# Performance work log

Measured on AMD Instinct MI355X. Metric: run time of the kernel, lower is better.

The kernel has to match this reference:

```python
import jax, jax.numpy as jnp
import numpy as np

WINDOW = 128
LOOK_BACKWARD = 1
LOOK_FORWARD = 0
PAD_VALUE = -1


def look_around(x, backward=LOOK_BACKWARD, forward=LOOK_FORWARD, pad_value=PAD_VALUE):
    # x: [b, windows, window_size, ...]; pad along windows axis, concat along window_size axis
    pad_width = [(0, 0)] * x.ndim
    pad_width[1] = (backward, forward)
    px = jnp.pad(x, pad_width, constant_values=pad_value)
    w = x.shape[1]
    return jnp.concatenate([px[:, i:i + w] for i in range(forward + backward + 1)], axis=2)


def rotate_half(x):
    x1, x2 = jnp.split(x, 2, axis=-1)
    return jnp.concatenate([-x2, x1], axis=-1)


def setup_inputs() -> dict:
    key = jax.random.key(0)
    k1, k2, k3 = jax.random.split(key, 3)
    B, H, N, D = 4, 16, 4096, 64
    return {
        "q": jax.random.normal(k1, (B, H, N, D), dtype=jnp.float32),
        "k": jax.random.normal(k2, (B, H, N, D), dtype=jnp.float32),
        "v": jax.random.normal(k3, (B, H, N, D), dtype=jnp.float32),
    }


def reference(q, k, v):
    B, H, N, D = q.shape
    qf = q.reshape(B * H, N, D)
    kf = k.reshape(B * H, N, D)
    vf = v.reshape(B * H, N, D)

    # --- inline rotary (SinusoidalEmbeddings + apply_rotary_pos_emb) ---
    inv_freq = 1.0 / (10000.0 ** (jnp.arange(0, D, 2, dtype=jnp.float32) / D))  # [D/2]
    t = jnp.arange(N, dtype=jnp.float32)
    half = t[:, None] * inv_freq[None, :]                      # [N, D/2]
    freqs = jnp.concatenate([half, half], axis=-1)             # [N, D]
    cos, sin = jnp.cos(freqs), jnp.sin(freqs)
    qf = qf * cos + rotate_half(qf) * sin
    kf = kf * cos + rotate_half(kf) * sin

    # --- blocked local attention ---
    w = WINDOW
    windows = N // w
    scale = D ** -0.5
    bq = qf.reshape(B * H, windows, w, D)
    bk = look_around(kf.reshape(B * H, windows, w, D))         # [bh, windows, j, D]
    bv = look_around(vf.reshape(B * H, windows, w, D))

    seq = jnp.arange(N).reshape(1, windows, w)
    bq_t = seq[..., :, None]                                   # [1, windows, w, 1]
    bq_k = look_around(seq)[..., None, :]                      # [1, windows, 1, j]

    sim = jnp.einsum('bwie,bwje->bwij', bq, bk) * scale        # [bh, windows, w, j]
    mask_value = -jnp.finfo(sim.dtype).max
    sim = jnp.where(bq_t < bq_k, mask_value, sim)              # causal mask

    attn = jax.nn.softmax(sim, axis=-1)
    out = jnp.einsum('bwij,bwje->bwie', attn, bv)              # [bh, windows, w, D]
    return out.reshape(B, H, N, D)
```

## Files before the change

### kernel.cpp

```cpp
#include <hip/hip_runtime.h>

typedef __attribute__((ext_vector_type(8))) short  short8;
typedef __attribute__((ext_vector_type(4))) short  short4v;
typedef __attribute__((ext_vector_type(4))) float  float4v;

#define MFMA_QK(A,B,C) __builtin_amdgcn_mfma_f32_16x16x32_bf16(A,B,C,0,0,0)
#define MFMA_PV(A,B,C) __builtin_amdgcn_mfma_f32_16x16x16bf16_1k(A,B,C,0,0,0)

static __device__ __forceinline__ short f2bf(float x) {
  unsigned u = __float_as_uint(x);
  u += 0x7fffu + ((u >> 16) & 1u);
  return (short)(u >> 16);
}

static __device__ __forceinline__ void rope_sc(float rev, float& sn, float& cs) {
  float fr = rev - floorf(rev);
  sn = __builtin_amdgcn_sinf(fr);
  cs = __builtin_amdgcn_cosf(fr);
}

static __device__ __forceinline__ float invfreq_rev(int idx) {
  return exp2f(-0.41524101186092034f * (float)idx) * 0.15915494309189535f;
}

#define N_ 4096
#define D_ 64
#define W_ 128

__global__ __launch_bounds__(512, 4)
void la_fused(const float* __restrict__ qg, const float* __restrict__ kg,
              const float* __restrict__ vg, float* __restrict__ outg)
{
  __shared__ __attribute__((aligned(16))) short Kl[256][72];
  __shared__ __attribute__((aligned(16))) short Vl[64][260];

  const int blk  = blockIdx.x;
  const int w    = blk & 31;
  const int bh   = blk >> 5;
  const int base = bh * (N_ * D_);
  const int tid  = threadIdx.x;

  {
    const float* kb = kg + base;
    const float* vb = vg + base;
#pragma unroll
    for (int it = 0; it < 4; ++it) {
      const int tau = it * 512 + tid;
      const int j   = tau >> 3;
      const int d0  = (tau & 7) << 2;
      const int g   = w * W_ - W_ + j;
      float klo[4], khi[4], vlo[4], vhi[4];
      if (g < 0) {
#pragma unroll
        for (int dd = 0; dd < 4; ++dd) { klo[dd]=khi[dd]=vlo[dd]=vhi[dd] = -1.0f; }
      } else {
        float4v a   = *(const float4v*)(kb + g * D_ + d0);
        float4v b   = *(const float4v*)(kb + g * D_ + d0 + 32);
        float4v va  = *(const float4v*)(vb + g * D_ + d0);
        float4v vb2 = *(const float4v*)(vb + g * D_ + d0 + 32);
        const float t = (float)g;
#pragma unroll
        for (int dd = 0; dd < 4; ++dd) {
          float sn, cs; rope_sc(t * invfreq_rev(d0 + dd), sn, cs);
          klo[dd] = a[dd] * cs - b[dd] * sn;
          khi[dd] = b[dd] * cs + a[dd] * sn;
          vlo[dd] = va[dd]; vhi[dd] = vb2[dd];
        }
      }
      short4v k0 = { f2bf(klo[0]), f2bf(klo[1]), f2bf(klo[2]), f2bf(klo[3]) };
      short4v k1 = { f2bf(khi[0]), f2bf(khi[1]), f2bf(khi[2]), f2bf(khi[3]) };
      *(short4v*)&Kl[j][d0]      = k0;
      *(short4v*)&Kl[j][d0 + 32] = k1;
      const int j4  = j >> 2;
      const int jlo = j & 3;
#pragma unroll
      for (int dd = 0; dd < 4; ++dd) {
        const int r0 = d0 + dd, r1 = r0 + 32;
        Vl[r0][((j4 ^ (r0 >> 4)) << 2) | jlo] = f2bf(vlo[dd]);
        Vl[r1][((j4 ^ (r1 >> 4)) << 2) | jlo] = f2bf(vhi[dd]);
      }
    }
  }
  __syncthreads();

  const int lane = tid & 63;
  const int wv   = tid >> 6;
  const int il   = lane & 15;
  const int qd   = lane >> 4;
  const int rw   = wv * 16 + il;

  short8 qf0, qf1;
  {
    const int n = w * W_ + rw;
    const float* qr = qg + base + n * D_ + qd * 8;
    float4v x0 = *(const float4v*)(qr);
    float4v x1 = *(const float4v*)(qr + 4);
    float4v y0 = *(const float4v*)(qr + 32);
    float4v y1 = *(const float4v*)(qr + 36);
    float lo[8], hi[8];
    const float t = (float)n;
#pragma unroll
    for (int jj = 0; jj < 8; ++jj) {
      const int d = qd * 8 + jj;
      float xx = (jj < 4) ? x0[jj & 3] : x1[jj & 3];
      float yy = (jj < 4) ? y0[jj & 3] : y1[jj & 3];
      float sn, cs; rope_sc(t * invfreq_rev(d), sn, cs);
      lo[jj] = xx * cs - yy * sn;
      hi[jj] = yy * cs + xx * sn;
    }
    qf0 = short8{ f2bf(lo[0]),f2bf(lo[1]),f2bf(lo[2]),f2bf(lo[3]),
                  f2bf(lo[4]),f2bf(lo[5]),f2bf(lo[6]),f2bf(lo[7]) };
    qf1 = short8{ f2bf(hi[0]),f2bf(hi[1]),f2bf(hi[2]),f2bf(hi[3]),
                  f2bf(hi[4]),f2bf(hi[5]),f2bf(hi[6]),f2bf(hi[7]) };
  }

  float4v O[4];
#pragma unroll
  for (int dt = 0; dt < 4; ++dt) { float4v z = {0.f,0.f,0.f,0.f}; O[dt] = z; }
  float sum = 0.f;
  const int tq = wv + 9;

#pragma unroll
  for (int t = 0; t < 16; ++t) if (t < tq) {
    const short8 a0 = *(const short8*)&Kl[t * 16 + il][qd * 8];
    const short8 a1 = *(const short8*)&Kl[t * 16 + il][32 + qd * 8];
    float4v S = {0.f, 0.f, 0.f, 0.f};
    S = MFMA_QK(a0, qf0, S);
    S = MFMA_QK(a1, qf1, S);
    float p[4];
#pragma unroll
    for (int r = 0; r < 4; ++r) {
      const int j = t * 16 + qd * 4 + r;
      float e = __expf(S[r] * 0.125f);
      p[r] = (j > rw + 128) ? 0.f : e;
      sum += p[r];
    }
    const short4v Pt = short4v{ f2bf(p[0]), f2bf(p[1]), f2bf(p[2]), f2bf(p[3]) };
    short4v af[4];
#pragma unroll
    for (int dt = 0; dt < 4; ++dt)
      af[dt] = *(const short4v*)&Vl[dt * 16 + il][((t * 4 + qd) ^ dt) << 2];
#pragma unroll
    for (int dt = 0; dt < 4; ++dt)
      O[dt] = MFMA_PV(af[dt], Pt, O[dt]);
  }

  sum += __shfl_xor(sum, 16);
  sum += __shfl_xor(sum, 32);
  const float inv = 1.0f / sum;

  float* op = outg + base + (w * W_ + rw) * D_;
#pragma unroll
  for (int dt = 0; dt < 4; ++dt) {
    float4v o = O[dt];
    o[0] *= inv; o[1] *= inv; o[2] *= inv; o[3] *= inv;
    *(float4v*)(op + dt * 16 + qd * 4) = o;
  }
}

extern "C" void kernel_launch(void* const* d_in, const int* in_sizes, int n_in,
                              void* d_out, int out_size, void* d_ws, size_t ws_size,
                              hipStream_t stream)
{
  const float* q = (const float*)d_in[0];
  const float* k = (const float*)d_in[1];
  const float* v = (const float*)d_in[2];
  float* out = (float*)d_out;
  la_fused<<<dim3(64 * 32), dim3(512), 0, stream>>>(q, k, v, out);
}
```

Before: 219.9 us.

## Precompute RoPE sin/cos table and halve LDS by staging K/V windows

Adds a small kernel that writes a cos/sin table for every position into the workspace, so the attention kernel reads rotary factors instead of evaluating transcendentals for each element. The attention kernel now stages the previous and current K/V windows one at a time in half-sized LDS buffers, with an extra barrier between them, and raises launch bounds to 8 blocks per CU to allow higher occupancy. The trade-offs are an extra kernel launch, extra global reads of the table, and serialised load/compute phases. If the workspace is too small, the kernel falls back to computing sin/cos inline.

New measurement: 282.7 us. 1.29x slower.

```diff
diff --git a/kernel.cpp b/kernel.cpp
--- a/kernel.cpp
+++ b/kernel.cpp
@@ -26,63 +26,38 @@
 #define N_ 4096
 #define D_ 64
 #define W_ 128
-
-__global__ __launch_bounds__(512, 4)
+#define TAB_BYTES ((size_t)N_ * 64 * sizeof(float))
+
+__global__ __launch_bounds__(256) void rope_table(float* __restrict__ tab) {
+  const int i  = blockIdx.x * 256 + threadIdx.x;
+  const int n  = i >> 3;
+  const int d0 = (i & 7) << 2;
+  float4v cs, sn;
+#pragma unroll
+  for (int dd = 0; dd < 4; ++dd) {
+    float fr = (float)n * invfreq_rev(d0 + dd);
+    fr -= floorf(fr);
+    cs[dd] = __builtin_amdgcn_cosf(fr);
+    sn[dd] = __builtin_amdgcn_sinf(fr);
+  }
+  *(float4v*)(tab + n * 64 + d0)      = cs;
+  *(float4v*)(tab + n * 64 + 32 + d0) = sn;
+}
+
+template<int USE_TABLE>
+__global__ __launch_bounds__(512, 8)
 void la_fused(const float* __restrict__ qg, const float* __restrict__ kg,
-              const float* __restrict__ vg, float* __restrict__ outg)
+              const float* __restrict__ vg, float* __restrict__ outg,
+              const float* __restrict__ tab)
 {
-  __shared__ __attribute__((aligned(16))) short Kl[256][72];
-  __shared__ __attribute__((aligned(16))) short Vl[64][260];
+  __shared__ __attribute__((aligned(16))) short Kl[128][72];
+  __shared__ __attribute__((aligned(16))) short Vl[64][130];
 
   const int blk  = blockIdx.x;
   const int w    = blk & 31;
   const int bh   = blk >> 5;
   const int base = bh * (N_ * D_);
   const int tid  = threadIdx.x;
-
-  {
-    const float* kb = kg + base;
-    const float* vb = vg + base;
-#pragma unroll
-    for (int it = 0; it < 4; ++it) {
-      const int tau = it * 512 + tid;
-      const int j   = tau >> 3;
-      const int d0  = (tau & 7) << 2;
-      const int g   = w * W_ - W_ + j;
-      float klo[4], khi[4], vlo[4], vhi[4];
-      if (g < 0) {
-#pragma unroll
-        for (int dd = 0; dd < 4; ++dd) { klo[dd]=khi[dd]=vlo[dd]=vhi[dd] = -1.0f; }
-      } else {
-        float4v a   = *(const float4v*)(kb + g * D_ + d0);
-        float4v b   = *(const float4v*)(kb + g * D_ + d0 + 32);
-        float4v va  = *(const float4v*)(vb + g * D_ + d0);
-        float4v vb2 = *(const float4v*)(vb + g * D_ + d0 + 32);
-        const float t = (float)g;
-#pragma unroll
-        for (int dd = 0; dd < 4; ++dd) {
-          float sn, cs; rope_sc(t * invfreq_rev(d0 + dd), sn, cs);
-          klo[dd] = a[dd] * cs - b[dd] * sn;
-          khi[dd] = b[dd] * cs + a[dd] * sn;
-          vlo[dd] = va[dd]; vhi[dd] = vb2[dd];
-        }
-      }
-      short4v k0 = { f2bf(klo[0]), f2bf(klo[1]), f2bf(klo[2]), f2bf(klo[3]) };
-      short4v k1 = { f2bf(khi[0]), f2bf(khi[1]), f2bf(khi[2]), f2bf(khi[3]) };
-      *(short4v*)&Kl[j][d0]      = k0;
-      *(short4v*)&Kl[j][d0 + 32] = k1;
-      const int j4  = j >> 2;
-      const int jlo = j & 3;
-#pragma unroll
-      for (int dd = 0; dd < 4; ++dd) {
-        const int r0 = d0 + dd, r1 = r0 + 32;
-        Vl[r0][((j4 ^ (r0 >> 4)) << 2) | jlo] = f2bf(vlo[dd]);
-        Vl[r1][((j4 ^ (r1 >> 4)) << 2) | jlo] = f2bf(vhi[dd]);
-      }
-    }
-  }
-  __syncthreads();
-
   const int lane = tid & 63;
   const int wv   = tid >> 6;
   const int il   = lane & 15;
@@ -98,15 +73,32 @@
     float4v y0 = *(const float4v*)(qr + 32);
     float4v y1 = *(const float4v*)(qr + 36);
     float lo[8], hi[8];
-    const float t = (float)n;
-#pragma unroll
-    for (int jj = 0; jj < 8; ++jj) {
-      const int d = qd * 8 + jj;
-      float xx = (jj < 4) ? x0[jj & 3] : x1[jj & 3];
-      float yy = (jj < 4) ? y0[jj & 3] : y1[jj & 3];
-      float sn, cs; rope_sc(t * invfreq_rev(d), sn, cs);
-      lo[jj] = xx * cs - yy * sn;
-      hi[jj] = yy * cs + xx * sn;
+    if (USE_TABLE) {
+      const float* tr = tab + n * 64 + qd * 8;
+      float4v c0 = *(const float4v*)(tr);
+      float4v c1 = *(const float4v*)(tr + 4);
+      float4v s0 = *(const float4v*)(tr + 32);
+      float4v s1 = *(const float4v*)(tr + 36);
+#pragma unroll
+      for (int jj = 0; jj < 8; ++jj) {
+        float xx = (jj < 4) ? x0[jj & 3] : x1[jj & 3];
+        float yy = (jj < 4) ? y0[jj & 3] : y1[jj & 3];
+        float cs = (jj < 4) ? c0[jj & 3] : c1[jj & 3];
+        float sn = (jj < 4) ? s0[jj & 3] : s1[jj & 3];
+        lo[jj] = xx * cs - yy * sn;
+        hi[jj] = yy * cs + xx * sn;
+      }
+    } else {
+      const float t = (float)n;
+#pragma unroll
+      for (int jj = 0; jj < 8; ++jj) {
+        const int d = qd * 8 + jj;
+        float xx = (jj < 4) ? x0[jj & 3] : x1[jj & 3];
+        float yy = (jj < 4) ? y0[jj & 3] : y1[jj & 3];
+        float sn, cs; rope_sc(t * invfreq_rev(d), sn, cs);
+        lo[jj] = xx * cs - yy * sn;
+        hi[jj] = yy * cs + xx * sn;
+      }
     }
     qf0 = short8{ f2bf(lo[0]),f2bf(lo[1]),f2bf(lo[2]),f2bf(lo[3]),
                   f2bf(lo[4]),f2bf(lo[5]),f2bf(lo[6]),f2bf(lo[7]) };
@@ -118,31 +110,90 @@
 #pragma unroll
   for (int dt = 0; dt < 4; ++dt) { float4v z = {0.f,0.f,0.f,0.f}; O[dt] = z; }
   float sum = 0.f;
-  const int tq = wv + 9;
-
-#pragma unroll
-  for (int t = 0; t < 16; ++t) if (t < tq) {
-    const short8 a0 = *(const short8*)&Kl[t * 16 + il][qd * 8];
-    const short8 a1 = *(const short8*)&Kl[t * 16 + il][32 + qd * 8];
-    float4v S = {0.f, 0.f, 0.f, 0.f};
-    S = MFMA_QK(a0, qf0, S);
-    S = MFMA_QK(a1, qf1, S);
-    float p[4];
-#pragma unroll
-    for (int r = 0; r < 4; ++r) {
-      const int j = t * 16 + qd * 4 + r;
-      float e = __expf(S[r] * 0.125f);
-      p[r] = (j > rw + 128) ? 0.f : e;
-      sum += p[r];
+
+  const float* kb = kg + base;
+  const float* vb = vg + base;
+
+#pragma unroll
+  for (int h = 0; h < 2; ++h) {
+    if (h) __syncthreads();
+
+#pragma unroll
+    for (int it = 0; it < 2; ++it) {
+      const int tau = it * 512 + tid;
+      const int j   = tau >> 3;
+      const int d0  = (tau & 7) << 2;
+      const int g   = (w - 1 + h) * W_ + j;
+      float klo[4], khi[4], vlo[4], vhi[4];
+      if (g < 0) {
+#pragma unroll
+        for (int dd = 0; dd < 4; ++dd) { klo[dd]=khi[dd]=vlo[dd]=vhi[dd] = -1.0f; }
+      } else {
+        float4v a   = *(const float4v*)(kb + g * D_ + d0);
+        float4v b   = *(const float4v*)(kb + g * D_ + d0 + 32);
+        float4v va  = *(const float4v*)(vb + g * D_ + d0);
+        float4v vb2 = *(const float4v*)(vb + g * D_ + d0 + 32);
+        if (USE_TABLE) {
+          float4v cs4 = *(const float4v*)(tab + g * 64 + d0);
+          float4v sn4 = *(const float4v*)(tab + g * 64 + 32 + d0);
+#pragma unroll
+          for (int dd = 0; dd < 4; ++dd) {
+            klo[dd] = a[dd] * cs4[dd] - b[dd] * sn4[dd];
+            khi[dd] = b[dd] * cs4[dd] + a[dd] * sn4[dd];
+            vlo[dd] = va[dd]; vhi[dd] = vb2[dd];
+          }
+        } else {
+          const float t = (float)g;
+#pragma unroll
+          for (int dd = 0; dd < 4; ++dd) {
+            float sn, cs; rope_sc(t * invfreq_rev(d0 + dd), sn, cs);
+            klo[dd] = a[dd] * cs - b[dd] * sn;
+            khi[dd] = b[dd] * cs + a[dd] * sn;
+            vlo[dd] = va[dd]; vhi[dd] = vb2[dd];
+          }
+        }
+      }
+      short4v k0 = { f2bf(klo[0]), f2bf(klo[1]), f2bf(klo[2]), f2bf(klo[3]) };
+      short4v k1 = { f2bf(khi[0]), f2bf(khi[1]), f2bf(khi[2]), f2bf(khi[3]) };
+      *(short4v*)&Kl[j][d0]      = k0;
+      *(short4v*)&Kl[j][d0 + 32] = k1;
+      const int j4  = j >> 2;
+      const int jlo = j & 3;
+#pragma unroll
+      for (int dd = 0; dd < 4; ++dd) {
+        const int r0 = d0 + dd, r1 = r0 + 32;
+        Vl[r0][((j4 ^ (r0 >> 4)) << 2) | jlo] = f2bf(vlo[dd]);
+        Vl[r1][((j4 ^ (r1 >> 4)) << 2) | jlo] = f2bf(vhi[dd]);
+      }
     }
-    const short4v Pt = short4v{ f2bf(p[0]), f2bf(p[1]), f2bf(p[2]), f2bf(p[3]) };
-    short4v af[4];
-#pragma unroll
-    for (int dt = 0; dt < 4; ++dt)
-      af[dt] = *(const short4v*)&Vl[dt * 16 + il][((t * 4 + qd) ^ dt) << 2];
-#pragma unroll
-    for (int dt = 0; dt < 4; ++dt)
-      O[dt] = MFMA_PV(af[dt], Pt, O[dt]);
+    __syncthreads();
+
+    const int tq = h ? (wv + 1) : 8;
+#pragma unroll
+    for (int t = 0; t < 8; ++t) if (t < tq) {
+      const int tt = h * 8 + t;
+      const short8 a0 = *(const short8*)&Kl[t * 16 + il][qd * 8];
+      const short8 a1 = *(const short8*)&Kl[t * 16 + il][32 + qd * 8];
+      float4v S = {0.f, 0.f, 0.f, 0.f};
+      S = MFMA_QK(a0, qf0, S);
+      S = MFMA_QK(a1, qf1, S);
+      float p[4];
+#pragma unroll
+      for (int r = 0; r < 4; ++r) {
+        const int j = tt * 16 + qd * 4 + r;
+        float e = __expf(S[r] * 0.125f);
+        p[r] = (j > rw + 128) ? 0.f : e;
+        sum += p[r];
+      }
+      const short4v Pt = short4v{ f2bf(p[0]), f2bf(p[1]), f2bf(p[2]), f2bf(p[3]) };
+      short4v af[4];
+#pragma unroll
+      for (int dt = 0; dt < 4; ++dt)
+        af[dt] = *(const short4v*)&Vl[dt * 16 + il][((t * 4 + qd) ^ dt) << 2];
+#pragma unroll
+      for (int dt = 0; dt < 4; ++dt)
+        O[dt] = MFMA_PV(af[dt], Pt, O[dt]);
+    }
   }
 
   sum += __shfl_xor(sum, 16);
@@ -166,5 +217,11 @@
   const float* k = (const float*)d_in[1];
   const float* v = (const float*)d_in[2];
   float* out = (float*)d_out;
-  la_fused<<<dim3(64 * 32), dim3(512), 0, stream>>>(q, k, v, out);
-}
+  float* tab = (float*)d_ws;
+  if (ws_size >= TAB_BYTES) {
+    rope_table<<<dim3(128), dim3(256), 0, stream>>>(tab);
+    la_fused<1><<<dim3(64 * 32), dim3(512), 0, stream>>>(q, k, v, out, tab);
+  } else {
+    la_fused<0><<<dim3(64 * 32), dim3(512), 0, stream>>>(q, k, v, out, nullptr);
+  }
+}
```
